# Performance work log

Measured on AMD Instinct MI355X. Metric: run time of the kernel, lower is better.

## Reference

```python
import jax, jax.numpy as jnp
import numpy as np
from itertools import combinations

TEMPERATURE = 0.1
EPS = 1e-8  # matches torch F.cosine_similarity eps

B, D = 4096, 512

def setup_inputs() -> dict:
    key = jax.random.key(0)
    k0, k1, k2 = jax.random.split(key, 3)
    return {
        "z0": jax.random.normal(k0, (B, D), dtype=jnp.float32),
        "z1": jax.random.normal(k1, (B, D), dtype=jnp.float32),
        "z2": jax.random.normal(k2, (B, D), dtype=jnp.float32),
    }

def _normalize(z):
    # cosine_similarity(a,b) == dot(a_hat, b_hat) with norms clamped at eps
    n = jnp.sqrt(jnp.sum(z * z, axis=-1, keepdims=True))
    return z / jnp.maximum(n, EPS)

def _ce(logits):
    # cross entropy with labels = arange(B): -log_softmax(logits)[i, i], mean over rows
    lse = jax.nn.logsumexp(logits, axis=1)          # [B]
    diag = jnp.diagonal(logits)                     # [B]
    return jnp.mean(lse - diag)

def reference(z0, z1, z2):
    latents = [z0, z1, z2]
    normed = [_normalize(z) for z in latents]
    pairs = list(combinations(range(len(latents)), 2))
    total = jnp.asarray(0.0, dtype=z0.dtype)
    for i, j in pairs:
        sim = jnp.einsum("bd,cd->bc", normed[i], normed[j]) / TEMPERATURE  # [B,B]
        total = total + ( _ce(sim) + _ce(sim.T) ) / 2
    return total / max(len(pairs), 1)
```

## Files before the change

### kernel.cpp

```cpp
#include <hip/hip_runtime.h>
#include <hip/hip_bf16.h>

#define NB 4096
#define ND 512

typedef int i32x4 __attribute__((ext_vector_type(4)));
typedef int i32x8 __attribute__((ext_vector_type(8)));
typedef float f32x4 __attribute__((ext_vector_type(4)));

#define AS1 __attribute__((address_space(1)))
#define AS3 __attribute__((address_space(3)))

__device__ __forceinline__ unsigned int f2e4m3(float x) {
    float a = fabsf(x);
    unsigned s = (__float_as_uint(x) >> 24) & 0x80u;
    if (a < 0.015625f) {
        int q = __float2int_rn(a * 512.0f);
        return s | (unsigned)q;
    }
    unsigned u = __float_as_uint(a);
    u += 0x7FFFFu + ((u >> 20) & 1u);
    unsigned e8 = (u >> 23) - 120u;
    unsigned m = (u >> 20) & 7u;
    return s | (e8 << 3) | m;
}

__global__ __launch_bounds__(256) void nrm_kernel(
    const float* __restrict__ z0, const float* __restrict__ z1,
    const float* __restrict__ z2, unsigned char* __restrict__ nrm8,
    float* __restrict__ rowsum, float* __restrict__ colsum)
{
    const int w = threadIdx.x >> 6, lane = threadIdx.x & 63;
    const int row = blockIdx.x * 4 + w;
    const int p = blockIdx.y;
    if (lane == 0) {
        rowsum[p * NB + row] = 0.f;
        colsum[p * NB + row] = 0.f;
    }
    const float* z = (p == 0) ? z0 : (p == 1) ? z1 : z2;
    const float4* zr = (const float4*)(z + (size_t)row * ND);
    const float4 a = zr[lane * 2], b = zr[lane * 2 + 1];
    float ss = a.x * a.x + a.y * a.y + a.z * a.z + a.w * a.w
             + b.x * b.x + b.y * b.y + b.z * b.z + b.w * b.w;
    #pragma unroll
    for (int m = 32; m >= 1; m >>= 1) ss += __shfl_xor(ss, m);
    const float inv = 1.0f / fmaxf(sqrtf(ss), 1e-8f);
    uint2 o;
    o.x = f2e4m3(a.x * inv) | (f2e4m3(a.y * inv) << 8)
        | (f2e4m3(a.z * inv) << 16) | (f2e4m3(a.w * inv) << 24);
    o.y = f2e4m3(b.x * inv) | (f2e4m3(b.y * inv) << 8)
        | (f2e4m3(b.z * inv) << 16) | (f2e4m3(b.w * inv) << 24);
    *(uint2*)(nrm8 + ((size_t)p * NB + row) * ND + lane * 8) = o;
}

__global__ __launch_bounds__(256, 2) void pair_gemm_kernel(
    const unsigned char* __restrict__ nrm8,
    float* __restrict__ rowsum, float* __restrict__ colsum,
    float* __restrict__ diag)
{
    const int bid = blockIdx.x;
    const int bxc = bid & 7;
    const int r = bid >> 3;
    const int p = r >> 5;
    const int by = r & 31;
    const int ia = (p == 2) ? 1 : 0;
    const int ib = (p == 0) ? 1 : 2;

    const char* Ag = (const char*)nrm8 + ((size_t)ia * NB + (size_t)by * 128) * ND;
    const char* Bg = (const char*)nrm8 + ((size_t)ib * NB + (size_t)bxc * 512) * ND;

    __shared__ char lds[65536];

    const int tid = threadIdx.x;
    const int lane = tid & 63;
    const int w = tid >> 6;
    const int wr = w >> 1, wc = w & 1;
    const int lr = lane & 15, lg = lane >> 4;

    int srcOff[4];
    #pragma unroll
    for (int q = 0; q < 4; ++q) {
        const int c = q * 256 + tid;
        const int rr = c >> 3;
        srcOff[q] = rr * ND + (((c & 7) ^ (rr & 7)) * 16);
    }

    const int s0 = ((2 * lg) ^ (lr & 7)) * 16;
    const int s1 = ((2 * lg + 1) ^ (lr & 7)) * 16;
    int arow[4], brow[4];
    #pragma unroll
    for (int m = 0; m < 4; ++m) {
        arow[m] = (wr * 64 + m * 16 + lr) * 128;
        brow[m] = (wc * 64 + m * 16 + lr) * 128;
    }

    f32x4 acc[4][4] = {};
    float rs[4][4];
    #pragma unroll
    for (int m = 0; m < 4; ++m)
        #pragma unroll
        for (int j = 0; j < 4; ++j) rs[m][j] = 0.f;

    #define STAGE(gsrc, dstbase) do {                                               \
        _Pragma("unroll")                                                           \
        for (int q = 0; q < 4; ++q)                                                 \
            __builtin_amdgcn_global_load_lds(                                       \
                (const AS1 void*)((gsrc) + srcOff[q]),                              \
                (AS3 void*)(lds + (dstbase) + q * 4096 + tid * 16), 16, 0, 0);      \
    } while (0)

    #define LDF(dst, base) do {                                                     \
        i32x4 lo_ = *(const i32x4*)((base) + s0);                                   \
        i32x4 hi_ = *(const i32x4*)((base) + s1);                                   \
        dst = __builtin_shufflevector(lo_, hi_, 0, 1, 2, 3, 4, 5, 6, 7);            \
    } while (0)

    #define SC 0x7F7F7F7F
    constexpr float C10 = 14.42695040888963f;

    STAGE(Ag, 0);
    STAGE(Bg, 32768);
    asm volatile("s_waitcnt vmcnt(0)" ::: "memory");
    __builtin_amdgcn_s_barrier();

    #pragma unroll 1
    for (int s = 0; s < 16; ++s) {
        const int bxl = s >> 2, k = s & 3;
        const int pb = s & 1;

        if (s < 15) {
            const int s1i = s + 1;
            const int po = s1i & 1;
            STAGE(Ag + (s1i & 3) * 128, po * 16384);
            STAGE(Bg + (size_t)(s1i >> 2) * 128 * ND + (s1i & 3) * 128,
                  32768 + po * 16384);
        }

        const char* ab = lds + pb * 16384;
        const char* bb = lds + 32768 + pb * 16384;
        i32x8 af[4], bf[4];
        #pragma unroll
        for (int m = 0; m < 4; ++m) LDF(af[m], ab + arow[m]);
        #pragma unroll
        for (int n = 0; n < 4; ++n) LDF(bf[n], bb + brow[n]);

        __builtin_amdgcn_s_setprio(1);
        #pragma unroll
        for (int m = 0; m < 4; ++m)
            #pragma unroll
            for (int n = 0; n < 4; ++n)
                acc[m][n] = __builtin_amdgcn_mfma_scale_f32_16x16x128_f8f6f4(
                    af[m], bf[n], acc[m][n], 0, 0, 0, SC, 0, SC);
        __builtin_amdgcn_s_setprio(0);

        if (k == 3) {
            const int bxg = bxc * 4 + bxl;
            if (by == bxg && wr == wc) {
                #pragma unroll
                for (int m = 0; m < 4; ++m)
                    #pragma unroll
                    for (int j = 0; j < 4; ++j)
                        if (lr == lg * 4 + j)
                            diag[p * NB + by * 128 + wr * 64 + m * 16 + lr] = acc[m][m][j];
            }
            float cs[4] = {0.f, 0.f, 0.f, 0.f};
            #pragma unroll
            for (int m = 0; m < 4; ++m)
                #pragma unroll
                for (int n = 0; n < 4; ++n)
                    #pragma unroll
                    for (int j = 0; j < 4; ++j) {
                        float e = exp2f(fmaf(acc[m][n][j], C10, -C10));
                        rs[m][j] += e;
                        cs[n] += e;
                    }
            #pragma unroll
            for (int n = 0; n < 4; ++n) {
                float v = cs[n];
                v += __shfl_xor(v, 16);
                v += __shfl_xor(v, 32);
                if (lg == 0)
                    atomicAdd(&colsum[p * NB + bxg * 128 + wc * 64 + n * 16 + lr], v);
            }
            #pragma unroll
            for (int m = 0; m < 4; ++m)
                #pragma unroll
                for (int n = 0; n < 4; ++n)
                    acc[m][n] = (f32x4){0.f, 0.f, 0.f, 0.f};
        }

        if (s < 15) {
            asm volatile("s_waitcnt vmcnt(0)" ::: "memory");
            __builtin_amdgcn_s_barrier();
        }
    }
    #undef STAGE
    #undef LDF

    #pragma unroll
    for (int m = 0; m < 4; ++m)
        #pragma unroll
        for (int j = 0; j < 4; ++j) {
            float v = rs[m][j];
            v += __shfl_xor(v, 1);
            v += __shfl_xor(v, 2);
            v += __shfl_xor(v, 4);
            v += __shfl_xor(v, 8);
            if (lr == 0)
                atomicAdd(&rowsum[p * NB + by * 128 + wr * 64 + m * 16 + lg * 4 + j], v);
        }
}

__global__ __launch_bounds__(1024) void finalize_kernel(
    const float* __restrict__ rowsum, const float* __restrict__ colsum,
    const float* __restrict__ diag, float* __restrict__ out)
{
    float s = 0.f;
    for (int i = threadIdx.x; i < 3 * NB; i += 1024) {
        s += 0.5f * (logf(rowsum[i]) + logf(colsum[i])) + 10.0f - 10.0f * diag[i];
    }
    #pragma unroll
    for (int m = 32; m >= 1; m >>= 1) s += __shfl_xor(s, m);
    __shared__ float sw[16];
    if ((threadIdx.x & 63) == 0) sw[threadIdx.x >> 6] = s;
    __syncthreads();
    if (threadIdx.x == 0) {
        float t = 0.f;
        #pragma unroll
        for (int i = 0; i < 16; ++i) t += sw[i];
        out[0] = t * (1.0f / (3.0f * NB));
    }
}

extern "C" void kernel_launch(void* const* d_in, const int* in_sizes, int n_in,
                              void* d_out, int out_size, void* d_ws, size_t ws_size,
                              hipStream_t stream) {
    const float* z0 = (const float*)d_in[0];
    const float* z1 = (const float*)d_in[1];
    const float* z2 = (const float*)d_in[2];
    float* out = (float*)d_out;

    char* ws = (char*)d_ws;
    unsigned char* nrm8 = (unsigned char*)ws;
    const size_t nrm_bytes = (size_t)3 * NB * ND;
    float* rowsum = (float*)(ws + nrm_bytes);
    float* colsum = rowsum + 3 * NB;
    float* diag = colsum + 3 * NB;

    nrm_kernel<<<dim3(NB / 4, 3), 256, 0, stream>>>(z0, z1, z2, nrm8, rowsum, colsum);
    pair_gemm_kernel<<<768, 256, 0, stream>>>(nrm8, rowsum, colsum, diag);
    finalize_kernel<<<1, 1024, 0, stream>>>(rowsum, colsum, diag, out);
}
```

Baseline: 65.96 us.

## Triple-buffer LDS with register double-buffered fragments, narrower B tile, parallel finalize

```diff
diff --git a/kernel.cpp b/kernel.cpp
--- a/kernel.cpp
+++ b/kernel.cpp
@@ -69,7 +69,7 @@
     const char* Ag = (const char*)nrm8 + ((size_t)ia * NB + (size_t)by * 128) * ND;
     const char* Bg = (const char*)nrm8 + ((size_t)ib * NB + (size_t)bxc * 512) * ND;
 
-    __shared__ char lds[65536];
+    __shared__ char lds[73728];
 
     const int tid = threadIdx.x;
     const int lane = tid & 63;
@@ -77,36 +77,48 @@
     const int wr = w >> 1, wc = w & 1;
     const int lr = lane & 15, lg = lane >> 4;
 
-    int srcOff[4];
+    int srcOffA[4], srcOffB[2];
     #pragma unroll
     for (int q = 0; q < 4; ++q) {
         const int c = q * 256 + tid;
         const int rr = c >> 3;
-        srcOff[q] = rr * ND + (((c & 7) ^ (rr & 7)) * 16);
+        srcOffA[q] = rr * ND + (((c & 7) ^ (rr & 7)) * 16);
+    }
+    #pragma unroll
+    for (int q = 0; q < 2; ++q) {
+        const int c = q * 256 + tid;
+        const int rr = c >> 3;
+        srcOffB[q] = rr * ND + (((c & 7) ^ (rr & 7)) * 16);
     }
 
     const int s0 = ((2 * lg) ^ (lr & 7)) * 16;
     const int s1 = ((2 * lg + 1) ^ (lr & 7)) * 16;
-    int arow[4], brow[4];
-    #pragma unroll
-    for (int m = 0; m < 4; ++m) {
-        arow[m] = (wr * 64 + m * 16 + lr) * 128;
-        brow[m] = (wc * 64 + m * 16 + lr) * 128;
-    }
-
-    f32x4 acc[4][4] = {};
+    int arow[4], brow[2];
+    #pragma unroll
+    for (int m = 0; m < 4; ++m) arow[m] = (wr * 64 + m * 16 + lr) * 128;
+    #pragma unroll
+    for (int n = 0; n < 2; ++n) brow[n] = (wc * 32 + n * 16 + lr) * 128;
+
+    f32x4 acc[4][2] = {};
     float rs[4][4];
     #pragma unroll
     for (int m = 0; m < 4; ++m)
         #pragma unroll
         for (int j = 0; j < 4; ++j) rs[m][j] = 0.f;
 
-    #define STAGE(gsrc, dstbase) do {                                               \
+    #define STAGE_A(ksl, dstbase) do {                                              \
         _Pragma("unroll")                                                           \
         for (int q = 0; q < 4; ++q)                                                 \
             __builtin_amdgcn_global_load_lds(                                       \
-                (const AS1 void*)((gsrc) + srcOff[q]),                              \
+                (const AS1 void*)(Ag + srcOffA[q] + (ksl) * 128),                   \
                 (AS3 void*)(lds + (dstbase) + q * 4096 + tid * 16), 16, 0, 0);      \
+    } while (0)
+    #define STAGE_B(bxl, ksl, dstbase) do {                                         \
+        _Pragma("unroll")                                                           \
+        for (int q = 0; q < 2; ++q)                                                 \
+            __builtin_amdgcn_global_load_lds(                                       \
+                (const AS1 void*)(Bg + (bxl) * 32768 + srcOffB[q] + (ksl) * 128),   \
+                (AS3 void*)(lds + 49152 + (dstbase) + q * 4096 + tid * 16), 16, 0, 0); \
     } while (0)
 
     #define LDF(dst, base) do {                                                     \
@@ -115,87 +127,119 @@
         dst = __builtin_shufflevector(lo_, hi_, 0, 1, 2, 3, 4, 5, 6, 7);            \
     } while (0)
 
+    #define LDFRAGS(afX, bfX, idx) do {                                             \
+        const char* aB_ = lds + (idx) * 16384;                                      \
+        const char* bB_ = lds + 49152 + (idx) * 8192;                               \
+        _Pragma("unroll")                                                           \
+        for (int m = 0; m < 4; ++m) LDF(afX[m], aB_ + arow[m]);                     \
+        _Pragma("unroll")                                                           \
+        for (int n = 0; n < 2; ++n) LDF(bfX[n], bB_ + brow[n]);                     \
+    } while (0)
+
     #define SC 0x7F7F7F7F
+    #define MFMA8(afX, bfX) do {                                                    \
+        __builtin_amdgcn_s_setprio(1);                                              \
+        _Pragma("unroll")                                                           \
+        for (int m = 0; m < 4; ++m)                                                 \
+            _Pragma("unroll")                                                       \
+            for (int n = 0; n < 2; ++n)                                             \
+                acc[m][n] = __builtin_amdgcn_mfma_scale_f32_16x16x128_f8f6f4(       \
+                    afX[m], bfX[n], acc[m][n], 0, 0, 0, SC, 0, SC);                 \
+        __builtin_amdgcn_s_setprio(0);                                              \
+    } while (0)
+
     constexpr float C10 = 14.42695040888963f;
 
-    STAGE(Ag, 0);
-    STAGE(Bg, 32768);
-    asm volatile("s_waitcnt vmcnt(0)" ::: "memory");
+    #define EPILOGUE(bxl) do {                                                      \
+        const int bxg_ = bxc * 8 + (bxl);                                           \
+        float cs_[2] = {0.f, 0.f};                                                  \
+        _Pragma("unroll")                                                           \
+        for (int m = 0; m < 4; ++m)                                                 \
+            _Pragma("unroll")                                                       \
+            for (int n = 0; n < 2; ++n)                                             \
+                _Pragma("unroll")                                                   \
+                for (int j = 0; j < 4; ++j) {                                       \
+                    float e = exp2f(fmaf(acc[m][n][j], C10, -C10));                 \
+                    rs[m][j] += e;                                                  \
+                    cs_[n] += e;                                                    \
+                }                                                                   \
+        if (bxg_ == by * 2 + wr) {                                                  \
+            _Pragma("unroll")                                                       \
+            for (int m = 0; m < 4; ++m) {                                           \
+                if (wc == (m >> 1) && lg == (lr >> 2)) {                            \
+                    f32x4 dv = acc[m][m & 1];                                       \
+                    const int jj = lr & 3;                                          \
+                    float val = (jj == 0) ? dv[0] : (jj == 1) ? dv[1]               \
+                              : (jj == 2) ? dv[2] : dv[3];                          \
+                    diag[p * NB + by * 128 + wr * 64 + m * 16 + lr] = val;          \
+                }                                                                   \
+            }                                                                       \
+        }                                                                           \
+        _Pragma("unroll")                                                           \
+        for (int n = 0; n < 2; ++n) {                                               \
+            float v = cs_[n];                                                       \
+            v += __shfl_xor(v, 16);                                                 \
+            v += __shfl_xor(v, 32);                                                 \
+            if (lg == 0)                                                            \
+                atomicAdd(&colsum[p * NB + bxg_ * 64 + wc * 32 + n * 16 + lr], v);  \
+        }                                                                           \
+        _Pragma("unroll")                                                           \
+        for (int m = 0; m < 4; ++m)                                                 \
+            _Pragma("unroll")                                                       \
+            for (int n = 0; n < 2; ++n)                                             \
+                acc[m][n] = (f32x4){0.f, 0.f, 0.f, 0.f};                            \
+    } while (0)
+
+    STAGE_A(0, 0);           STAGE_B(0, 0, 0);
+    STAGE_A(1, 16384);       STAGE_B(0, 1, 8192);
+    asm volatile("s_waitcnt vmcnt(6)" ::: "memory");
     __builtin_amdgcn_s_barrier();
 
+    i32x8 afA[4], bfA[2], afB[4], bfB[2];
+    LDFRAGS(afA, bfA, 0);
+
+    int idxL = 1;
+    int idxS = 2;
+
     #pragma unroll 1
-    for (int s = 0; s < 16; ++s) {
-        const int bxl = s >> 2, k = s & 3;
-        const int pb = s & 1;
-
-        if (s < 15) {
-            const int s1i = s + 1;
-            const int po = s1i & 1;
-            STAGE(Ag + (s1i & 3) * 128, po * 16384);
-            STAGE(Bg + (size_t)(s1i >> 2) * 128 * ND + (s1i & 3) * 128,
-                  32768 + po * 16384);
+    for (int tt = 0; tt < 16; ++tt) {
+        {
+            const int s2 = 2 * tt + 2;
+            if (tt < 15) {
+                STAGE_A(s2 & 3, idxS * 16384);
+                STAGE_B(s2 >> 2, s2 & 3, idxS * 8192);
+            }
+            if (tt == 15)           asm volatile("s_waitcnt vmcnt(0) lgkmcnt(0)" ::: "memory");
+            else if (tt > 0 && (tt & 1) == 0)
+                                    asm volatile("s_waitcnt vmcnt(8) lgkmcnt(0)" ::: "memory");
+            else                    asm volatile("s_waitcnt vmcnt(6) lgkmcnt(0)" ::: "memory");
+            __builtin_amdgcn_s_barrier();
+            LDFRAGS(afB, bfB, idxL);
+            MFMA8(afA, bfA);
+            idxL = (idxL == 2) ? 0 : idxL + 1;
+            idxS = (idxS == 2) ? 0 : idxS + 1;
         }
-
-        const char* ab = lds + pb * 16384;
-        const char* bb = lds + 32768 + pb * 16384;
-        i32x8 af[4], bf[4];
-        #pragma unroll
-        for (int m = 0; m < 4; ++m) LDF(af[m], ab + arow[m]);
-        #pragma unroll
-        for (int n = 0; n < 4; ++n) LDF(bf[n], bb + brow[n]);
-
-        __builtin_amdgcn_s_setprio(1);
-        #pragma unroll
-        for (int m = 0; m < 4; ++m)
-            #pragma unroll
-            for (int n = 0; n < 4; ++n)
-                acc[m][n] = __builtin_amdgcn_mfma_scale_f32_16x16x128_f8f6f4(
-                    af[m], bf[n], acc[m][n], 0, 0, 0, SC, 0, SC);
-        __builtin_amdgcn_s_setprio(0);
-
-        if (k == 3) {
-            const int bxg = bxc * 4 + bxl;
-            if (by == bxg && wr == wc) {
-                #pragma unroll
-                for (int m = 0; m < 4; ++m)
-                    #pragma unroll
-                    for (int j = 0; j < 4; ++j)
-                        if (lr == lg * 4 + j)
-                            diag[p * NB + by * 128 + wr * 64 + m * 16 + lr] = acc[m][m][j];
+        {
+            const int s2 = 2 * tt + 3;
+            if (tt < 15) {
+                STAGE_A(s2 & 3, idxS * 16384);
+                STAGE_B(s2 >> 2, s2 & 3, idxS * 8192);
+                asm volatile("s_waitcnt vmcnt(6) lgkmcnt(0)" ::: "memory");
+                __builtin_amdgcn_s_barrier();
+                LDFRAGS(afA, bfA, idxL);
             }
-            float cs[4] = {0.f, 0.f, 0.f, 0.f};
-            #pragma unroll
-            for (int m = 0; m < 4; ++m)
-                #pragma unroll
-                for (int n = 0; n < 4; ++n)
-                    #pragma unroll
-                    for (int j = 0; j < 4; ++j) {
-                        float e = exp2f(fmaf(acc[m][n][j], C10, -C10));
-                        rs[m][j] += e;
-                        cs[n] += e;
-                    }
-            #pragma unroll
-            for (int n = 0; n < 4; ++n) {
-                float v = cs[n];
-                v += __shfl_xor(v, 16);
-                v += __shfl_xor(v, 32);
-                if (lg == 0)
-                    atomicAdd(&colsum[p * NB + bxg * 128 + wc * 64 + n * 16 + lr], v);
-            }
-            #pragma unroll
-            for (int m = 0; m < 4; ++m)
-                #pragma unroll
-                for (int n = 0; n < 4; ++n)
-                    acc[m][n] = (f32x4){0.f, 0.f, 0.f, 0.f};
+            MFMA8(afB, bfB);
+            if (tt & 1) EPILOGUE(tt >> 1);
+            idxL = (idxL == 2) ? 0 : idxL + 1;
+            idxS = (idxS == 2) ? 0 : idxS + 1;
         }
-
-        if (s < 15) {
-            asm volatile("s_waitcnt vmcnt(0)" ::: "memory");
-            __builtin_amdgcn_s_barrier();
-        }
-    }
-    #undef STAGE
+    }
+    #undef STAGE_A
+    #undef STAGE_B
     #undef LDF
+    #undef LDFRAGS
+    #undef MFMA8
+    #undef EPILOGUE
 
     #pragma unroll
     for (int m = 0; m < 4; ++m)
@@ -211,25 +255,19 @@
         }
 }
 
-__global__ __launch_bounds__(1024) void finalize_kernel(
+__global__ __launch_bounds__(256) void finalize_kernel(
     const float* __restrict__ rowsum, const float* __restrict__ colsum,
     const float* __restrict__ diag, float* __restrict__ out)
 {
-    float s = 0.f;
-    for (int i = threadIdx.x; i < 3 * NB; i += 1024) {
-        s += 0.5f * (logf(rowsum[i]) + logf(colsum[i])) + 10.0f - 10.0f * diag[i];
-    }
+    const int i = blockIdx.x * 256 + threadIdx.x;
+    float s = 0.5f * (logf(rowsum[i]) + logf(colsum[i])) + 10.0f - 10.0f * diag[i];
     #pragma unroll
     for (int m = 32; m >= 1; m >>= 1) s += __shfl_xor(s, m);
-    __shared__ float sw[16];
+    __shared__ float sw[4];
     if ((threadIdx.x & 63) == 0) sw[threadIdx.x >> 6] = s;
     __syncthreads();
-    if (threadIdx.x == 0) {
-        float t = 0.f;
-        #pragma unroll
-        for (int i = 0; i < 16; ++i) t += sw[i];
-        out[0] = t * (1.0f / (3.0f * NB));
-    }
+    if (threadIdx.x == 0)
+        atomicAdd(out, (sw[0] + sw[1] + sw[2] + sw[3]) * (1.0f / (3.0f * NB)));
 }
 
 extern "C" void kernel_launch(void* const* d_in, const int* in_sizes, int n_in,
@@ -247,7 +285,8 @@
     float* colsum = rowsum + 3 * NB;
     float* diag = colsum + 3 * NB;
 
+    hipMemsetAsync(out, 0, sizeof(float), stream);
     nrm_kernel<<<dim3(NB / 4, 3), 256, 0, stream>>>(z0, z1, z2, nrm8, rowsum, colsum);
     pair_gemm_kernel<<<768, 256, 0, stream>>>(nrm8, rowsum, colsum, diag);
-    finalize_kernel<<<1, 1024, 0, stream>>>(rowsum, colsum, diag, out);
-}
+    finalize_kernel<<<48, 256, 0, stream>>>(rowsum, colsum, diag, out);
+}
```

After: 80.93 us. 22.7% more time.
